# Kernel optimization log

Hardware: AMD Instinct MI355X
Metric: run time of the kernel (lower is better)

## Reference

```python
import jax, jax.numpy as jnp
import numpy as np

T, H, F, E, K, C = 8192, 1024, 2048, 16, 2, 1280  # tokens, hidden, ffn, experts, top_k, capacity


def setup_inputs() -> dict:
    key = jax.random.key(0)
    ks = jax.random.split(key, 6)
    return {
        "x": jax.random.normal(ks[0], (T, H), dtype=jnp.float32),
        "w_router": jax.random.normal(ks[1], (H, E), dtype=jnp.float32) * 0.02,
        "w1": jax.random.normal(ks[2], (E, H, F), dtype=jnp.float32) * 0.02,
        "b1": jnp.zeros((E, F), dtype=jnp.float32),
        "w2": jax.random.normal(ks[3], (E, F, H), dtype=jnp.float32) * 0.02,
        "b2": jnp.zeros((E, H), dtype=jnp.float32),
    }


def reference(x, w_router, w1, b1, w2, b2):
    # ---- Router: softmax + top-k (TopKRouter) ----
    logits = x @ w_router                                  # [T, E]
    probs = jax.nn.softmax(logits, axis=-1)
    topk_p, topk_idx = jax.lax.top_k(probs, K)             # [T, K]
    topk_p = topk_p / jnp.sum(topk_p, axis=-1, keepdims=True)

    # ---- Dispatch with capacity drop (token_permutation) ----
    flat_e = topk_idx.reshape(-1)                          # [T*K] expert id per assignment
    token_ids = jnp.repeat(jnp.arange(T), K)               # [T*K]
    oh = jax.nn.one_hot(flat_e, E, dtype=jnp.int32)        # [T*K, E]
    # position of each assignment within its expert's buffer (token order)
    pos = jnp.cumsum(oh, axis=0) - oh                      # [T*K, E]
    pos = jnp.take_along_axis(pos, flat_e[:, None], axis=1)[:, 0]  # [T*K]
    keep = pos < C
    safe_pos = jnp.where(keep, pos, C)                     # dropped tokens -> dummy slot C

    dispatched = jnp.zeros((E, C + 1, H), dtype=x.dtype)
    dispatched = dispatched.at[flat_e, safe_pos].add(x[token_ids])
    disp = dispatched[:, :C, :]                            # [E, C, H]

    # ---- Grouped expert MLP (SequentialMLP: fc1 -> gelu -> fc2) ----
    h = jax.nn.gelu(jnp.einsum("ech,ehf->ecf", disp, w1) + b1[:, None, :])
    y = jnp.einsum("ecf,efh->ech", h, w2) + b2[:, None, :]  # [E, C, H]

    # ---- Combine (token_unpermutation): gather + prob-weighted sum ----
    y_pad = jnp.pad(y, ((0, 0), (0, 1), (0, 0)))            # dummy slot returns garbage, masked below
    gathered = y_pad[flat_e, safe_pos]                      # [T*K, H]
    gathered = jnp.where(keep[:, None], gathered, 0.0)
    weighted = gathered * topk_p.reshape(-1)[:, None]
    out = jax.ops.segment_sum(weighted, token_ids, num_segments=T)  # [T, H]
    return out
```

## Files before the change

### kernel.cpp

```cpp
#include <hip/hip_runtime.h>
#include <cstdint>
#include <cstddef>

#define T_TOK 8192
#define HDIM  1024
#define FDIM  2048
#define NEXP  16
#define CAP   1280

typedef __bf16 bf16x8 __attribute__((ext_vector_type(8)));
typedef float  f32x4  __attribute__((ext_vector_type(4)));

__device__ inline void gld16(const void* g, void* l) {
  __builtin_amdgcn_global_load_lds(
      (__attribute__((address_space(1))) void*)g,
      (__attribute__((address_space(3))) void*)l, 16, 0, 0);
}

__global__ __launch_bounds__(256) void router_kernel(
    const float* __restrict__ x, const float* __restrict__ wr,
    int* __restrict__ eidx, float* __restrict__ eprob) {
  int t = blockIdx.x * 4 + (threadIdx.x >> 6);
  int lane = threadIdx.x & 63;
  float acc[NEXP];
#pragma unroll
  for (int e = 0; e < NEXP; ++e) acc[e] = 0.f;
  const float4* xp = (const float4*)(x + (size_t)t * HDIM + lane * 16);
#pragma unroll
  for (int q = 0; q < 4; ++q) {
    float4 xv = xp[q];
    float xa[4] = {xv.x, xv.y, xv.z, xv.w};
#pragma unroll
    for (int ii = 0; ii < 4; ++ii) {
      int h = lane * 16 + q * 4 + ii;
      const float4* wp = (const float4*)(wr + (size_t)h * NEXP);
      float w[NEXP];
      float4 w0 = wp[0], w1 = wp[1], w2 = wp[2], w3 = wp[3];
      w[0]=w0.x; w[1]=w0.y; w[2]=w0.z; w[3]=w0.w;
      w[4]=w1.x; w[5]=w1.y; w[6]=w1.z; w[7]=w1.w;
      w[8]=w2.x; w[9]=w2.y; w[10]=w2.z; w[11]=w2.w;
      w[12]=w3.x; w[13]=w3.y; w[14]=w3.z; w[15]=w3.w;
#pragma unroll
      for (int e = 0; e < NEXP; ++e) acc[e] += xa[ii] * w[e];
    }
  }
#pragma unroll
  for (int e = 0; e < NEXP; ++e) {
#pragma unroll
    for (int s = 32; s > 0; s >>= 1) acc[e] += __shfl_xor(acc[e], s);
  }
  if (lane == 0) {
    float l0 = -1e30f, l1 = -1e30f; int i0 = 0, i1 = 0;
#pragma unroll
    for (int e = 0; e < NEXP; ++e) {
      float v = acc[e];
      if (v > l0) { l1 = l0; i1 = i0; l0 = v; i0 = e; }
      else if (v > l1) { l1 = v; i1 = e; }
    }
    float p0 = 1.f / (1.f + __expf(l1 - l0));
    eidx[t * 2 + 0] = i0; eidx[t * 2 + 1] = i1;
    eprob[t * 2 + 0] = p0; eprob[t * 2 + 1] = 1.f - p0;
  }
}

__global__ __launch_bounds__(256) void pos_kernel(
    const int* __restrict__ eidx, const float* __restrict__ eprob,
    int* __restrict__ slot_token, float* __restrict__ slot_prob) {
  __shared__ int scan[256][NEXP];
  int tid = threadIdx.x;
  int cnt[NEXP];
#pragma unroll
  for (int e = 0; e < NEXP; ++e) cnt[e] = 0;
  int base_i = tid * 64;
  const int4* ep = (const int4*)(eidx + base_i);
  for (int i = 0; i < 16; ++i) {
    int4 v = ep[i];
    cnt[v.x]++; cnt[v.y]++; cnt[v.z]++; cnt[v.w]++;
  }
#pragma unroll
  for (int e = 0; e < NEXP; ++e) scan[tid][e] = cnt[e];
  __syncthreads();
  if (tid < NEXP) {
    int run = 0;
    for (int i = 0; i < 256; ++i) { int v = scan[i][tid]; scan[i][tid] = run; run += v; }
  }
  __syncthreads();
  int basec[NEXP];
#pragma unroll
  for (int e = 0; e < NEXP; ++e) basec[e] = scan[tid][e];
  for (int i = 0; i < 64; ++i) {
    int fi = base_i + i;
    int e = eidx[fi];
    int p = basec[e]++;
    if (p < CAP) {
      slot_token[e * CAP + p] = fi >> 1;
      slot_prob[e * CAP + p] = eprob[fi];
    }
  }
}

__global__ __launch_bounds__(256) void scatter_kernel(
    const float* __restrict__ x, const int* __restrict__ slot_token,
    __bf16* __restrict__ disp) {
  int s = blockIdx.x * 4 + (threadIdx.x >> 6);
  int lane = threadIdx.x & 63;
  int e = s / CAP, m = s % CAP;
  int tok = slot_token[s];
  __bf16 vals[16] __attribute__((aligned(16)));
  if (tok >= 0) {
    const float4* xp = (const float4*)(x + (size_t)tok * HDIM + lane * 16);
#pragma unroll
    for (int q = 0; q < 4; ++q) {
      float4 v = xp[q];
      vals[q * 4 + 0] = (__bf16)v.x; vals[q * 4 + 1] = (__bf16)v.y;
      vals[q * 4 + 2] = (__bf16)v.z; vals[q * 4 + 3] = (__bf16)v.w;
    }
  } else {
#pragma unroll
    for (int q = 0; q < 16; ++q) vals[q] = (__bf16)0.f;
  }
  uint4* dst = (uint4*)(disp + (((size_t)e * 16 + (lane >> 2)) * CAP + m) * 64 + (lane & 3) * 16);
  dst[0] = ((uint4*)vals)[0];
  dst[1] = ((uint4*)vals)[1];
}

__global__ __launch_bounds__(256) void transpose_cast_kernel(
    const float* __restrict__ src, __bf16* __restrict__ dst, int R, int Cc) {
  int e = blockIdx.z;
  src += (size_t)e * R * Cc;
  dst += (size_t)e * R * Cc;
  __shared__ float tile[64][65];
  int gy = blockIdx.y * 64;
  int gx = blockIdx.x * 64;
  int tid = threadIdx.x;
  int r = tid >> 4;
  int c4 = (tid & 15) * 4;
#pragma unroll
  for (int rr = 0; rr < 4; ++rr) {
    float4 v = *(const float4*)(src + (size_t)(gy + r + rr * 16) * Cc + gx + c4);
    tile[r + rr * 16][c4 + 0] = v.x;
    tile[r + rr * 16][c4 + 1] = v.y;
    tile[r + rr * 16][c4 + 2] = v.z;
    tile[r + rr * 16][c4 + 3] = v.w;
  }
  __syncthreads();
  int r2 = tid >> 2;
  int cb = (tid & 3) * 16;
  __bf16 o[16] __attribute__((aligned(16)));
#pragma unroll
  for (int i = 0; i < 16; ++i) o[i] = (__bf16)tile[cb + i][r2];
  uint4* dp = (uint4*)(dst + ((size_t)(gy >> 6) * Cc + gx + r2) * 64 + cb);
  dp[0] = ((uint4*)o)[0];
  dp[1] = ((uint4*)o)[1];
}

template <int EPI, int KSPLIT>
__global__ __launch_bounds__(512, 2) void moe_gemm_kernel(
    const __bf16* __restrict__ A, const __bf16* __restrict__ Bt,
    const float* __restrict__ bias, __bf16* __restrict__ Hout,
    const int* __restrict__ slot_token, const float* __restrict__ slot_prob,
    float* __restrict__ out, int M, int N, int Kd) {
  const int nwg = gridDim.x * gridDim.y * gridDim.z;
  int flat = (blockIdx.z * gridDim.y + blockIdx.y) * gridDim.x + blockIdx.x;
  flat = (flat & 7) * (nwg >> 3) + (flat >> 3);
  const int bx = flat % gridDim.x;
  int tmpf = flat / gridDim.x;
  const int by = tmpf % gridDim.y;
  const int bz = tmpf / gridDim.y;

  const int e  = bz / KSPLIT;
  const int ks = bz % KSPLIT;
  const int m0 = by * 256, n0 = bx * 256;
  __shared__ __bf16 lds[2 * 32768];
  const int tid = threadIdx.x, wave = tid >> 6, lane = tid & 63;
  const int quad = lane >> 4, l15 = lane & 15;
  const int wm = (wave >> 2) * 128, wn = (wave & 3) * 64;
  f32x4 acc[8][4] = {};
  const int ktiles = (Kd / KSPLIT) >> 6;
  const size_t slabA = (size_t)M * 128;
  const size_t slabB = (size_t)N * 128;

  const int rbase = tid >> 3;
  const int swz = ((tid & 7) ^ (rbase & 7)) * 16;
  const char* srcA = (const char*)A + (size_t)e * (Kd >> 6) * slabA
                     + (size_t)(m0 + rbase) * 128 + swz;
  const char* srcB = (const char*)Bt + (size_t)e * (Kd >> 6) * slabB
                     + (size_t)(n0 + rbase) * 128 + swz;
  const int dofs = tid * 16;

  auto stage = [&](int t) {
    char* base = (char*)lds + (t & 1) * 65536;
    const char* sA = srcA + (size_t)(ks * ktiles + t) * slabA;
    const char* sB = srcB + (size_t)(ks * ktiles + t) * slabB;
#pragma unroll
    for (int j = 0; j < 4; ++j)
      gld16(sA + j * 8192, base + dofs + j * 8192);
#pragma unroll
    for (int j = 0; j < 4; ++j)
      gld16(sB + j * 8192, base + 32768 + dofs + j * 8192);
  };

  int aoff[8], boff[4], coff[2];
#pragma unroll
  for (int i = 0; i < 8; ++i) aoff[i] = (wm + i * 16 + l15) * 128;
#pragma unroll
  for (int j = 0; j < 4; ++j) boff[j] = (wn + j * 16 + l15) * 128;
#pragma unroll
  for (int kk = 0; kk < 2; ++kk) coff[kk] = (((kk * 4 + quad) ^ (l15 & 7)) * 16);

  stage(0);
  __builtin_amdgcn_s_waitcnt(0x0f70);
  __builtin_amdgcn_s_barrier();
  for (int t = 0; t < ktiles; ++t) {
    if (t + 1 < ktiles) stage(t + 1);
    const char* La = (const char*)lds + (t & 1) * 65536;
    const char* Lb = La + 32768;
#pragma unroll
    for (int kk = 0; kk < 2; ++kk) {
      bf16x8 av[8], bv[4];
#pragma unroll
      for (int i = 0; i < 8; ++i) av[i] = *(const bf16x8*)(La + aoff[i] + coff[kk]);
#pragma unroll
      for (int j = 0; j < 4; ++j) bv[j] = *(const bf16x8*)(Lb + boff[j] + coff[kk]);
      __builtin_amdgcn_s_setprio(1);
#pragma unroll
      for (int i = 0; i < 8; ++i)
#pragma unroll
        for (int j = 0; j < 4; ++j)
          acc[i][j] = __builtin_amdgcn_mfma_f32_16x16x32_bf16(av[i], bv[j], acc[i][j], 0, 0, 0);
      __builtin_amdgcn_s_setprio(0);
    }
    if (t + 1 < ktiles) __builtin_amdgcn_s_waitcnt(0x0f70);
    __builtin_amdgcn_s_barrier();
  }
  if (EPI == 1) {
    __bf16* He = Hout + (size_t)e * M * N;
    const size_t kfbase = (size_t)((n0 + wn) >> 6) * M;
    float bj[4];
#pragma unroll
    for (int j = 0; j < 4; ++j) bj[j] = bias[(size_t)e * N + n0 + wn + j * 16 + l15];
#pragma unroll
    for (int i = 0; i < 8; ++i) {
#pragma unroll
      for (int r = 0; r < 4; ++r) {
        int m = m0 + wm + i * 16 + quad * 4 + r;
#pragma unroll
        for (int j = 0; j < 4; ++j) {
          float v = acc[i][j][r] + bj[j];
          float u = 0.7978845608028654f * (v + 0.044715f * v * v * v);
          float ex = __expf(-2.f * fabsf(u));
          float th = (1.f - ex) / (1.f + ex);
          th = copysignf(th, u);
          He[(kfbase + m) * 64 + j * 16 + l15] = (__bf16)(0.5f * v * (1.f + th));
        }
      }
    }
  } else {
    const int* st = slot_token + e * CAP;
    const float* sp = slot_prob + e * CAP;
    float bj[4];
#pragma unroll
    for (int j = 0; j < 4; ++j)
      bj[j] = (ks == 0) ? bias[(size_t)e * N + n0 + wn + j * 16 + l15] : 0.f;
#pragma unroll
    for (int i = 0; i < 8; ++i) {
#pragma unroll
      for (int r = 0; r < 4; ++r) {
        int m = m0 + wm + i * 16 + quad * 4 + r;
        int tok = st[m];
        if (tok >= 0) {
          float p = sp[m];
#pragma unroll
          for (int j = 0; j < 4; ++j) {
            int n = n0 + wn + j * 16 + l15;
            float v = acc[i][j][r] + bj[j];
            atomicAdd(out + (size_t)tok * HDIM + n, p * v);
          }
        }
      }
    }
  }
}

extern "C" void kernel_launch(void* const* d_in, const int* in_sizes, int n_in,
                              void* d_out, int out_size, void* d_ws, size_t ws_size,
                              hipStream_t stream) {
  const float* x  = (const float*)d_in[0];
  const float* wr = (const float*)d_in[1];
  const float* w1 = (const float*)d_in[2];
  const float* b1 = (const float*)d_in[3];
  const float* w2 = (const float*)d_in[4];
  const float* b2 = (const float*)d_in[5];
  float* out = (float*)d_out;

  char* ws = (char*)d_ws;
  size_t off = 0;
  __bf16* w1t = (__bf16*)(ws + off); off += (size_t)NEXP * FDIM * HDIM * 2;
  __bf16* w2t = (__bf16*)(ws + off); off += (size_t)NEXP * HDIM * FDIM * 2;
  __bf16* disp = (__bf16*)(ws + off); off += (size_t)NEXP * CAP * HDIM * 2;
  __bf16* hbuf = (__bf16*)(ws + off); off += (size_t)NEXP * CAP * FDIM * 2;
  int*   slot_token = (int*)(ws + off);  off += (size_t)NEXP * CAP * 4;
  float* slot_prob  = (float*)(ws + off); off += (size_t)NEXP * CAP * 4;
  int*   eidx  = (int*)(ws + off);  off += (size_t)T_TOK * 2 * 4;
  float* eprob = (float*)(ws + off); off += (size_t)T_TOK * 2 * 4;
  if (ws_size < off) return;

  hipMemsetAsync(slot_token, 0xFF, (size_t)NEXP * CAP * 4, stream);
  hipMemsetAsync(d_out, 0, (size_t)T_TOK * HDIM * 4, stream);

  transpose_cast_kernel<<<dim3(FDIM / 64, HDIM / 64, NEXP), 256, 0, stream>>>(w1, w1t, HDIM, FDIM);
  transpose_cast_kernel<<<dim3(HDIM / 64, FDIM / 64, NEXP), 256, 0, stream>>>(w2, w2t, FDIM, HDIM);

  router_kernel<<<T_TOK / 4, 256, 0, stream>>>(x, wr, eidx, eprob);
  pos_kernel<<<1, 256, 0, stream>>>(eidx, eprob, slot_token, slot_prob);
  scatter_kernel<<<NEXP * CAP / 4, 256, 0, stream>>>(x, slot_token, disp);

  moe_gemm_kernel<1, 1><<<dim3(FDIM / 256, CAP / 256, NEXP), 512, 0, stream>>>(
      disp, w1t, b1, hbuf, nullptr, nullptr, nullptr, CAP, FDIM, HDIM);
  moe_gemm_kernel<2, 2><<<dim3(HDIM / 256, CAP / 256, NEXP * 2), 512, 0, stream>>>(
      hbuf, w2t, b2, nullptr, slot_token, slot_prob, out, CAP, HDIM, FDIM);
}
```

Measured before the change: 754.9 us.

## Triple-buffer GEMM with K=32 tiles and interleaved per-operand staging

The grouped GEMM moves from a double-buffered 64-wide K tile to a triple-buffered 32-wide K tile (96KB LDS instead of 128KB). Loads for tile t+2 are split per operand and issued between the two halves of the MFMA work, so global-to-LDS traffic overlaps compute more finely. The swizzle changes to match the narrower rows. The pos kernel also keeps its per-thread counters in LDS instead of register arrays, which avoids dynamically indexed register arrays that could spill to scratch. The extra barriers per iteration and the smaller K tile add synchronisation overhead.

```diff
diff --git a/kernel.cpp b/kernel.cpp
--- a/kernel.cpp
+++ b/kernel.cpp
@@ -68,30 +68,24 @@
     int* __restrict__ slot_token, float* __restrict__ slot_prob) {
   __shared__ int scan[256][NEXP];
   int tid = threadIdx.x;
-  int cnt[NEXP];
-#pragma unroll
-  for (int e = 0; e < NEXP; ++e) cnt[e] = 0;
+#pragma unroll
+  for (int e = 0; e < NEXP; ++e) scan[tid][e] = 0;
   int base_i = tid * 64;
   const int4* ep = (const int4*)(eidx + base_i);
   for (int i = 0; i < 16; ++i) {
     int4 v = ep[i];
-    cnt[v.x]++; cnt[v.y]++; cnt[v.z]++; cnt[v.w]++;
-  }
-#pragma unroll
-  for (int e = 0; e < NEXP; ++e) scan[tid][e] = cnt[e];
+    scan[tid][v.x]++; scan[tid][v.y]++; scan[tid][v.z]++; scan[tid][v.w]++;
+  }
   __syncthreads();
   if (tid < NEXP) {
     int run = 0;
     for (int i = 0; i < 256; ++i) { int v = scan[i][tid]; scan[i][tid] = run; run += v; }
   }
   __syncthreads();
-  int basec[NEXP];
-#pragma unroll
-  for (int e = 0; e < NEXP; ++e) basec[e] = scan[tid][e];
   for (int i = 0; i < 64; ++i) {
     int fi = base_i + i;
     int e = eidx[fi];
-    int p = basec[e]++;
+    int p = scan[tid][e]++;
     if (p < CAP) {
       slot_token[e * CAP + p] = fi >> 1;
       slot_prob[e * CAP + p] = eprob[fi];
@@ -171,68 +165,87 @@
   const int e  = bz / KSPLIT;
   const int ks = bz % KSPLIT;
   const int m0 = by * 256, n0 = bx * 256;
-  __shared__ __bf16 lds[2 * 32768];
+  __shared__ __bf16 lds[3 * 16384];
   const int tid = threadIdx.x, wave = tid >> 6, lane = tid & 63;
   const int quad = lane >> 4, l15 = lane & 15;
   const int wm = (wave >> 2) * 128, wn = (wave & 3) * 64;
   f32x4 acc[8][4] = {};
-  const int ktiles = (Kd / KSPLIT) >> 6;
+  const int ktiles = (Kd / KSPLIT) >> 5;
   const size_t slabA = (size_t)M * 128;
   const size_t slabB = (size_t)N * 128;
 
-  const int rbase = tid >> 3;
-  const int swz = ((tid & 7) ^ (rbase & 7)) * 16;
-  const char* srcA = (const char*)A + (size_t)e * (Kd >> 6) * slabA
-                     + (size_t)(m0 + rbase) * 128 + swz;
-  const char* srcB = (const char*)Bt + (size_t)e * (Kd >> 6) * slabB
-                     + (size_t)(n0 + rbase) * 128 + swz;
-  const int dofs = tid * 16;
-
-  auto stage = [&](int t) {
-    char* base = (char*)lds + (t & 1) * 65536;
-    const char* sA = srcA + (size_t)(ks * ktiles + t) * slabA;
-    const char* sB = srcB + (size_t)(ks * ktiles + t) * slabB;
-#pragma unroll
-    for (int j = 0; j < 4; ++j)
-      gld16(sA + j * 8192, base + dofs + j * 8192);
-#pragma unroll
-    for (int j = 0; j < 4; ++j)
-      gld16(sB + j * 8192, base + 32768 + dofs + j * 8192);
+  const int lrow0 = wave * 32 + (lane >> 2);
+  const int swz = ((lane & 3) ^ ((lane >> 3) & 3)) * 16;
+  const char* pA0 = (const char*)A + (size_t)e * (Kd >> 6) * slabA
+                    + (size_t)(m0 + lrow0) * 128 + swz;
+  const char* pB0 = (const char*)Bt + (size_t)e * (Kd >> 6) * slabB
+                    + (size_t)(n0 + lrow0) * 128 + swz;
+  const int dlo = wave * 2048 + lane * 16;
+  const int kgbase = ks * ktiles;
+
+  auto stage_op = [&](int t, int b, int isB) {
+    int kg = kgbase + t;
+    char* dst = (char*)lds + b * 32768 + isB * 16384 + dlo;
+    const char* s = (isB ? pB0 : pA0)
+                    + (size_t)(kg >> 1) * (isB ? slabB : slabA) + (kg & 1) * 64;
+    gld16(s,               dst);
+    gld16(s + 16 * 128,    dst + 1024);
   };
 
-  int aoff[8], boff[4], coff[2];
-#pragma unroll
-  for (int i = 0; i < 8; ++i) aoff[i] = (wm + i * 16 + l15) * 128;
-#pragma unroll
-  for (int j = 0; j < 4; ++j) boff[j] = (wn + j * 16 + l15) * 128;
-#pragma unroll
-  for (int kk = 0; kk < 2; ++kk) coff[kk] = (((kk * 4 + quad) ^ (l15 & 7)) * 16);
-
-  stage(0);
-  __builtin_amdgcn_s_waitcnt(0x0f70);
+  int aoff[8], boff[4];
+#pragma unroll
+  for (int i = 0; i < 8; ++i) aoff[i] = (wm + i * 16 + l15) * 64;
+#pragma unroll
+  for (int j = 0; j < 4; ++j) boff[j] = (wn + j * 16 + l15) * 64;
+  const int coff = ((quad ^ ((l15 >> 1) & 3)) * 16);
+
+  stage_op(0, 0, 0); stage_op(0, 0, 1);
+  if (ktiles > 1) { stage_op(1, 1, 0); stage_op(1, 1, 1); }
+  if (ktiles > 1) __builtin_amdgcn_s_waitcnt(0x0f74);
+  else            __builtin_amdgcn_s_waitcnt(0x0f70);
   __builtin_amdgcn_s_barrier();
+
+  int bcur = 0, bstage = 2;
   for (int t = 0; t < ktiles; ++t) {
-    if (t + 1 < ktiles) stage(t + 1);
-    const char* La = (const char*)lds + (t & 1) * 65536;
-    const char* Lb = La + 32768;
-#pragma unroll
-    for (int kk = 0; kk < 2; ++kk) {
-      bf16x8 av[8], bv[4];
-#pragma unroll
-      for (int i = 0; i < 8; ++i) av[i] = *(const bf16x8*)(La + aoff[i] + coff[kk]);
-#pragma unroll
-      for (int j = 0; j < 4; ++j) bv[j] = *(const bf16x8*)(Lb + boff[j] + coff[kk]);
-      __builtin_amdgcn_s_setprio(1);
-#pragma unroll
-      for (int i = 0; i < 8; ++i)
-#pragma unroll
-        for (int j = 0; j < 4; ++j)
-          acc[i][j] = __builtin_amdgcn_mfma_f32_16x16x32_bf16(av[i], bv[j], acc[i][j], 0, 0, 0);
-      __builtin_amdgcn_s_setprio(0);
-    }
-    if (t + 1 < ktiles) __builtin_amdgcn_s_waitcnt(0x0f70);
+    const char* La = (const char*)lds + bcur * 32768;
+    const char* Lb = La + 16384;
+    bf16x8 av[4], bv[4];
+#pragma unroll
+    for (int j = 0; j < 4; ++j) bv[j] = *(const bf16x8*)(Lb + boff[j] + coff);
+#pragma unroll
+    for (int i = 0; i < 4; ++i) av[i] = *(const bf16x8*)(La + aoff[i] + coff);
+    if (t + 2 < ktiles) stage_op(t + 2, bstage, 0);
     __builtin_amdgcn_s_barrier();
-  }
+    __builtin_amdgcn_s_waitcnt(0xc07f);
+    __builtin_amdgcn_s_setprio(1);
+#pragma unroll
+    for (int i = 0; i < 4; ++i)
+#pragma unroll
+      for (int j = 0; j < 4; ++j)
+        acc[i][j] = __builtin_amdgcn_mfma_f32_16x16x32_bf16(av[i], bv[j], acc[i][j], 0, 0, 0);
+    __builtin_amdgcn_s_setprio(0);
+    __builtin_amdgcn_s_barrier();
+#pragma unroll
+    for (int i = 0; i < 4; ++i) av[i] = *(const bf16x8*)(La + aoff[4 + i] + coff);
+    if (t + 2 < ktiles) stage_op(t + 2, bstage, 1);
+    __builtin_amdgcn_s_barrier();
+    __builtin_amdgcn_s_waitcnt(0xc07f);
+    __builtin_amdgcn_s_setprio(1);
+#pragma unroll
+    for (int i = 0; i < 4; ++i)
+#pragma unroll
+      for (int j = 0; j < 4; ++j)
+        acc[4 + i][j] = __builtin_amdgcn_mfma_f32_16x16x32_bf16(av[i], bv[j], acc[4 + i][j], 0, 0, 0);
+    __builtin_amdgcn_s_setprio(0);
+    if (t + 1 < ktiles) {
+      if (t + 2 < ktiles) __builtin_amdgcn_s_waitcnt(0x0f74);
+      else                __builtin_amdgcn_s_waitcnt(0x0f70);
+    }
+    __builtin_amdgcn_s_barrier();
+    bcur = (bcur == 2) ? 0 : bcur + 1;
+    bstage = (bstage == 2) ? 0 : bstage + 1;
+  }
+
   if (EPI == 1) {
     __bf16* He = Hout + (size_t)e * M * N;
     const size_t kfbase = (size_t)((n0 + wn) >> 6) * M;
```

Result: no change. 767.7 us (+1.7%).

## Shrink GEMM M-tile, triple-buffer A in LDS, load B directly into registers

Applied to the files above, without the earlier changes.

The grouped GEMM tile drops from 256x256 to 128x256, doubling the grid. Only A is staged through LDS, now in a three-deep ring, while each wave reads its B fragments straight from global memory into double-buffered registers one k-step ahead. The aim is less LDS traffic and footprint, more resident workgroups, and better overlap of loads with MFMA. In exchange, B is re-read from global memory by each wave row and register pressure rises. The pos_kernel also keeps its per-thread counters in shared memory instead of register arrays, avoiding dynamically indexed register arrays.

```diff
diff --git a/kernel.cpp b/kernel.cpp
--- a/kernel.cpp
+++ b/kernel.cpp
@@ -68,30 +68,24 @@
     int* __restrict__ slot_token, float* __restrict__ slot_prob) {
   __shared__ int scan[256][NEXP];
   int tid = threadIdx.x;
-  int cnt[NEXP];
-#pragma unroll
-  for (int e = 0; e < NEXP; ++e) cnt[e] = 0;
+#pragma unroll
+  for (int e = 0; e < NEXP; ++e) scan[tid][e] = 0;
   int base_i = tid * 64;
   const int4* ep = (const int4*)(eidx + base_i);
   for (int i = 0; i < 16; ++i) {
     int4 v = ep[i];
-    cnt[v.x]++; cnt[v.y]++; cnt[v.z]++; cnt[v.w]++;
-  }
-#pragma unroll
-  for (int e = 0; e < NEXP; ++e) scan[tid][e] = cnt[e];
+    scan[tid][v.x]++; scan[tid][v.y]++; scan[tid][v.z]++; scan[tid][v.w]++;
+  }
   __syncthreads();
   if (tid < NEXP) {
     int run = 0;
     for (int i = 0; i < 256; ++i) { int v = scan[i][tid]; scan[i][tid] = run; run += v; }
   }
   __syncthreads();
-  int basec[NEXP];
-#pragma unroll
-  for (int e = 0; e < NEXP; ++e) basec[e] = scan[tid][e];
   for (int i = 0; i < 64; ++i) {
     int fi = base_i + i;
     int e = eidx[fi];
-    int p = basec[e]++;
+    int p = scan[tid][e]++;
     if (p < CAP) {
       slot_token[e * CAP + p] = fi >> 1;
       slot_prob[e * CAP + p] = eprob[fi];
@@ -170,69 +164,82 @@
 
   const int e  = bz / KSPLIT;
   const int ks = bz % KSPLIT;
-  const int m0 = by * 256, n0 = bx * 256;
-  __shared__ __bf16 lds[2 * 32768];
+  const int m0 = by * 128, n0 = bx * 256;
+  __shared__ __bf16 lds[3 * 8192];
   const int tid = threadIdx.x, wave = tid >> 6, lane = tid & 63;
   const int quad = lane >> 4, l15 = lane & 15;
-  const int wm = (wave >> 2) * 128, wn = (wave & 3) * 64;
-  f32x4 acc[8][4] = {};
-  const int ktiles = (Kd / KSPLIT) >> 6;
+  const int wm = (wave >> 2) * 64, wn = (wave & 3) * 64;
+  f32x4 acc[4][4] = {};
+  const int kt = (Kd / KSPLIT) >> 6;
+  const int kgbase = ks * kt;
   const size_t slabA = (size_t)M * 128;
   const size_t slabB = (size_t)N * 128;
 
-  const int rbase = tid >> 3;
-  const int swz = ((tid & 7) ^ (rbase & 7)) * 16;
+  const int arow = tid >> 3;
+  const int aswz = ((tid & 7) ^ (arow & 7)) * 16;
   const char* srcA = (const char*)A + (size_t)e * (Kd >> 6) * slabA
-                     + (size_t)(m0 + rbase) * 128 + swz;
+                     + (size_t)(m0 + arow) * 128 + aswz;
+  char* const dstA = (char*)lds + tid * 16;
+
   const char* srcB = (const char*)Bt + (size_t)e * (Kd >> 6) * slabB
-                     + (size_t)(n0 + rbase) * 128 + swz;
-  const int dofs = tid * 16;
-
-  auto stage = [&](int t) {
-    char* base = (char*)lds + (t & 1) * 65536;
-    const char* sA = srcA + (size_t)(ks * ktiles + t) * slabA;
-    const char* sB = srcB + (size_t)(ks * ktiles + t) * slabB;
-#pragma unroll
-    for (int j = 0; j < 4; ++j)
-      gld16(sA + j * 8192, base + dofs + j * 8192);
-#pragma unroll
-    for (int j = 0; j < 4; ++j)
-      gld16(sB + j * 8192, base + 32768 + dofs + j * 8192);
+                     + (size_t)(n0 + wn + l15) * 128 + quad * 16;
+
+  auto stageA = [&](int t, int b) {
+    const char* s = srcA + (size_t)(kgbase + t) * slabA;
+    char* d = dstA + b * 16384;
+    gld16(s, d);
+    gld16(s + 8192, d + 8192);
   };
-
-  int aoff[8], boff[4], coff[2];
-#pragma unroll
-  for (int i = 0; i < 8; ++i) aoff[i] = (wm + i * 16 + l15) * 128;
-#pragma unroll
-  for (int j = 0; j < 4; ++j) boff[j] = (wn + j * 16 + l15) * 128;
-#pragma unroll
-  for (int kk = 0; kk < 2; ++kk) coff[kk] = (((kk * 4 + quad) ^ (l15 & 7)) * 16);
-
-  stage(0);
-  __builtin_amdgcn_s_waitcnt(0x0f70);
-  __builtin_amdgcn_s_barrier();
-  for (int t = 0; t < ktiles; ++t) {
-    if (t + 1 < ktiles) stage(t + 1);
-    const char* La = (const char*)lds + (t & 1) * 65536;
-    const char* Lb = La + 32768;
+  auto loadBV = [&](bf16x8 (&bv)[8], int t) {
+    const char* p = srcB + (size_t)(kgbase + t) * slabB;
+#pragma unroll
+    for (int j = 0; j < 4; ++j) {
+      bv[j]     = *(const bf16x8*)(p + j * 2048);
+      bv[4 + j] = *(const bf16x8*)(p + j * 2048 + 64);
+    }
+  };
+
+  int aoff[4], coff[2];
+#pragma unroll
+  for (int i = 0; i < 4; ++i) aoff[i] = (wm + i * 16 + l15) * 128;
+#pragma unroll
+  for (int kk = 0; kk < 2; ++kk) coff[kk] = ((kk * 4 + quad) ^ (l15 & 7)) * 16;
+
+  bf16x8 bv0[8], bv1[8];
+  stageA(0, 0);
+  loadBV(bv0, 0);
+  if (kt > 1) stageA(1, 1);
+
+  int bcur = 0, bstage = 2;
+  for (int t = 0; t < kt; ++t) {
+    bf16x8 (&bvC)[8] = (t & 1) ? bv1 : bv0;
+    bf16x8 (&bvN)[8] = (t & 1) ? bv0 : bv1;
+    if (t + 1 < kt) __builtin_amdgcn_s_waitcnt(0x0f72);
+    else            __builtin_amdgcn_s_waitcnt(0x0f70);
+    __builtin_amdgcn_s_barrier();
+    __builtin_amdgcn_sched_barrier(0);
+    if (t + 1 < kt) loadBV(bvN, t + 1);
+    __builtin_amdgcn_sched_barrier(0);
+    if (t + 2 < kt) stageA(t + 2, bstage);
+    __builtin_amdgcn_sched_barrier(0);
+    const char* La = (const char*)lds + bcur * 16384;
 #pragma unroll
     for (int kk = 0; kk < 2; ++kk) {
-      bf16x8 av[8], bv[4];
-#pragma unroll
-      for (int i = 0; i < 8; ++i) av[i] = *(const bf16x8*)(La + aoff[i] + coff[kk]);
-#pragma unroll
-      for (int j = 0; j < 4; ++j) bv[j] = *(const bf16x8*)(Lb + boff[j] + coff[kk]);
+      bf16x8 av[4];
+#pragma unroll
+      for (int i = 0; i < 4; ++i) av[i] = *(const bf16x8*)(La + aoff[i] + coff[kk]);
       __builtin_amdgcn_s_setprio(1);
 #pragma unroll
-      for (int i = 0; i < 8; ++i)
+      for (int i = 0; i < 4; ++i)
 #pragma unroll
         for (int j = 0; j < 4; ++j)
-          acc[i][j] = __builtin_amdgcn_mfma_f32_16x16x32_bf16(av[i], bv[j], acc[i][j], 0, 0, 0);
+          acc[i][j] = __builtin_amdgcn_mfma_f32_16x16x32_bf16(av[i], bvC[kk * 4 + j], acc[i][j], 0, 0, 0);
       __builtin_amdgcn_s_setprio(0);
     }
-    if (t + 1 < ktiles) __builtin_amdgcn_s_waitcnt(0x0f70);
-    __builtin_amdgcn_s_barrier();
-  }
+    bcur = (bcur == 2) ? 0 : bcur + 1;
+    bstage = (bstage == 2) ? 0 : bstage + 1;
+  }
+
   if (EPI == 1) {
     __bf16* He = Hout + (size_t)e * M * N;
     const size_t kfbase = (size_t)((n0 + wn) >> 6) * M;
@@ -240,7 +247,7 @@
 #pragma unroll
     for (int j = 0; j < 4; ++j) bj[j] = bias[(size_t)e * N + n0 + wn + j * 16 + l15];
 #pragma unroll
-    for (int i = 0; i < 8; ++i) {
+    for (int i = 0; i < 4; ++i) {
 #pragma unroll
       for (int r = 0; r < 4; ++r) {
         int m = m0 + wm + i * 16 + quad * 4 + r;
@@ -263,7 +270,7 @@
     for (int j = 0; j < 4; ++j)
       bj[j] = (ks == 0) ? bias[(size_t)e * N + n0 + wn + j * 16 + l15] : 0.f;
 #pragma unroll
-    for (int i = 0; i < 8; ++i) {
+    for (int i = 0; i < 4; ++i) {
 #pragma unroll
       for (int r = 0; r < 4; ++r) {
         int m = m0 + wm + i * 16 + quad * 4 + r;
@@ -315,8 +322,8 @@
   pos_kernel<<<1, 256, 0, stream>>>(eidx, eprob, slot_token, slot_prob);
   scatter_kernel<<<NEXP * CAP / 4, 256, 0, stream>>>(x, slot_token, disp);
 
-  moe_gemm_kernel<1, 1><<<dim3(FDIM / 256, CAP / 256, NEXP), 512, 0, stream>>>(
+  moe_gemm_kernel<1, 1><<<dim3(FDIM / 256, CAP / 128, NEXP), 512, 0, stream>>>(
       disp, w1t, b1, hbuf, nullptr, nullptr, nullptr, CAP, FDIM, HDIM);
-  moe_gemm_kernel<2, 2><<<dim3(HDIM / 256, CAP / 256, NEXP * 2), 512, 0, stream>>>(
+  moe_gemm_kernel<2, 2><<<dim3(HDIM / 256, CAP / 128, NEXP * 2), 512, 0, stream>>>(
       hbuf, w2t, b2, nullptr, slot_token, slot_prob, out, CAP, HDIM, FDIM);
 }
```

New measurement: 1.133 ms. +50.1%, slower.
